# Performance work log

Hardware: AMD Instinct MI355X
Metric: run time of the kernel (lower is better)

## Reference

```python
import jax, jax.numpy as jnp
from jax import lax
import numpy as np

KSIZE = 3
STRIDE = 1
PAD = 1
SOFTMAX_SCALE = 10.0
EPS = 1e-4


def _unfold(x, k, stride, pad):
    # x: [B, C, H, W] -> ([B, L, C, k, k], Ho, Wo)  (matches torch nn.Unfold ordering)
    B, C, H, W = x.shape
    xp = jnp.pad(x, ((0, 0), (0, 0), (pad, pad), (pad, pad)))
    Ho = (H + 2 * pad - k) // stride + 1
    Wo = (W + 2 * pad - k) // stride + 1
    cols = jnp.stack(
        [xp[:, :, i:i + Ho * stride:stride, j:j + Wo * stride:stride]
         for i in range(k) for j in range(k)], axis=2)  # [B, C, k*k, Ho, Wo]
    cols = cols.reshape(B, C, k, k, Ho * Wo)
    return cols.transpose(0, 4, 1, 2, 3), Ho, Wo


def setup_inputs() -> dict:
    key = jax.random.key(0)
    kb, kf, km = jax.random.split(key, 3)
    b = jax.random.normal(kb, (4, 64, 64, 64), dtype=jnp.float32)
    f = jax.random.normal(kf, (4, 64, 64, 64), dtype=jnp.float32)
    mask = jax.random.uniform(km, (4, 1, 256, 256), dtype=jnp.float32)
    return {"b": b, "f": f, "mask": mask}


def reference(b, f, mask):
    B, C, H, W = f.shape
    k = KSIZE
    # background patches: [B, L, C, k, k]
    bp, _, _ = _unfold(b, k, STRIDE, PAD)
    # mask: avg_pool2d(kernel=4, stride=mask_scale) with mask_scale = mask.W // f.W = 4
    mp = mask.reshape(B, 1, H, 4, W, 4).mean(axis=(3, 5))  # [B, 1, H, W]
    m_unf, _, _ = _unfold(mp, k, STRIDE, PAD)  # [B, L, 1, k, k]
    m0 = m_unf[0]  # quirk of original code: first sample's mask patches used for all
    w = bp * m0[None]  # masked background patches [B, L, C, k, k]
    f_masked = f * (1.0 - mp)
    # L2 norm over (C, k, k) per patch
    norm = jnp.sqrt(jnp.sum(w * w, axis=(2, 3, 4), keepdims=True) + EPS)
    wn = w / norm
    # cosine-similarity score: conv2d(f_masked, wn) as a GEMM over unfolded f
    fp, Ho, Wo = _unfold(f_masked, k, STRIDE, PAD)  # [B, Q, C, k, k]
    score = jnp.einsum('bqcij,blcij->blq', fp, wn).reshape(B, -1, Ho, Wo)  # [B, L, Ho, Wo]
    attn = jax.nn.softmax(score * SOFTMAX_SCALE, axis=1)
    offsets = jnp.argmax(score, axis=1)[:, None]  # [B, 1, Ho, Wo]
    # conv_transpose2d(attn, w, padding=1) == conv2d with spatially flipped, channel-swapped kernel
    pad_ct = k - 1 - 1

    def _ct(a, w_i):  # a: [L, Ho, Wo], w_i: [L, C, k, k]
        kern = jnp.flip(w_i, axis=(-2, -1)).transpose(1, 0, 2, 3)  # [C, L, k, k]
        return lax.conv_general_dilated(
            a[None], kern, (1, 1), [(pad_ct, pad_ct), (pad_ct, pad_ct)],
            dimension_numbers=('NCHW', 'OIHW', 'NCHW'))[0]

    y = jax.vmap(_ct)(attn, w)  # [B, C, Ho, Wo]
    return y, offsets
```

## Files before the change

### kernel.cpp

```cpp
#include <hip/hip_runtime.h>
#include <math.h>

typedef unsigned int u32;
typedef unsigned short u16;
typedef unsigned long long u64;
typedef _Float16 h8v __attribute__((ext_vector_type(8)));
typedef float f4v __attribute__((ext_vector_type(4)));
typedef u32 u4v __attribute__((ext_vector_type(4)));

#define B_ 4
#define C_ 64
#define HW 4096
#define L_ 4096
#define D_ 576
#define MW 256
#define SCALE 10.0f
#define EPS 1e-4f
#define TAU 0.015f
#define PAIRCAP 262144

__device__ __forceinline__ u16 f16b(float x) {
  union { _Float16 h; u16 u; } c; c.h = (_Float16)x; return c.u;
}
__device__ __forceinline__ float f16f(u16 v) {
  union { u16 u; _Float16 h; } c; c.u = v; return (float)c.h;
}

__device__ __forceinline__ void gld16(const void* g, void* l) {
  __builtin_amdgcn_global_load_lds((const __attribute__((address_space(1))) void*)g,
                                   (__attribute__((address_space(3))) void*)l, 16, 0, 0);
}

__global__ __launch_bounds__(256) void k_mp(const float* __restrict__ mask, float* __restrict__ mp) {
  int idx = blockIdx.x * 256 + threadIdx.x;
  int b = idx >> 12, p = idx & 4095;
  int y = p >> 6, x = p & 63;
  const float* mb = mask + (size_t)b * MW * MW;
  float s = 0.f;
  #pragma unroll
  for (int i = 0; i < 4; ++i)
    #pragma unroll
    for (int j = 0; j < 4; ++j)
      s += mb[(y * 4 + i) * MW + x * 4 + j];
  mp[idx] = s * (1.f / 16.f);
}

__global__ __launch_bounds__(256) void k_pre2(const float* __restrict__ f, const float* __restrict__ mp,
                                              float* __restrict__ m0, float* __restrict__ fm) {
  int blk = blockIdx.x;
  if (blk < 144) {
    int idx = blk * 256 + threadIdx.x;
    int l = idx / 9, t = idx - l * 9;
    int ly = l >> 6, lx = l & 63;
    int i = t / 3, j = t - i * 3;
    int yy = ly + i - 1, xx = lx + j - 1;
    float v = 0.f;
    if ((unsigned)yy < 64u && (unsigned)xx < 64u) v = mp[(yy << 6) + xx];
    m0[idx] = v;
  } else {
    int idx = (blk - 144) * 256 + threadIdx.x;
    int p = idx & 4095;
    int b = idx >> 18;
    fm[idx] = f[idx] * (1.f - mp[(b << 12) + p]);
  }
}

__device__ __forceinline__ float patch_val(const float* __restrict__ img, const float* __restrict__ m0,
                                           int l, int d) {
  int c = d / 9, t = d - c * 9;
  int ly = l >> 6, lx = l & 63;
  int i = t / 3, j = t - i * 3;
  int yy = ly + i - 1, xx = lx + j - 1;
  float v = 0.f;
  if ((unsigned)yy < 64u && (unsigned)xx < 64u) {
    v = img[(c << 12) + (yy << 6) + xx];
    if (m0) v *= m0[l * 9 + t];
  }
  return v;
}

__global__ __launch_bounds__(256) void k_prep(const float* __restrict__ bimg, const float* __restrict__ fmb,
                                              const float* __restrict__ m0,
                                              u16* __restrict__ w_h, u16* __restrict__ fp_h,
                                              u16* __restrict__ wT_h,
                                              double* __restrict__ norme, float* __restrict__ normv,
                                              int* __restrict__ rcount, int* __restrict__ pcount,
                                              u64* __restrict__ rbest) {
  int blk = blockIdx.x;
  if (blk < 4608) {
    int gid = blk * 256 + threadIdx.x;
    int idx = gid * 2;
    int l = idx / D_, d = idx - l * D_;
    u32 h0 = f16b(patch_val(bimg, m0, l, d));
    u32 h1 = f16b(patch_val(bimg, m0, l, d + 1));
    ((u32*)w_h)[gid] = h0 | (h1 << 16);
  } else if (blk < 5632) {
    int l = (blk - 4608) * 4 + (threadIdx.x >> 6);
    int lane = threadIdx.x & 63;
    int ly = l >> 6, lx = l & 63;
    double s = 0.0;
    for (int i = lane; i < D_; i += 64) {
      int c = i / 9, t = i - c * 9;
      int ii = t / 3, jj = t - ii * 3;
      int yy = ly + ii - 1, xx = lx + jj - 1;
      if ((unsigned)yy < 64u && (unsigned)xx < 64u) {
        float wv = bimg[(c << 12) + (yy << 6) + xx] * m0[l * 9 + t];
        s += (double)wv * (double)wv;
      }
    }
    #pragma unroll
    for (int off = 32; off; off >>= 1) s += __shfl_down(s, off);
    if (lane == 0) {
      double n = sqrt(s + (double)EPS);
      norme[l] = n; normv[l] = (float)n;
    }
  } else if (blk < 10752) {
    int gid = (blk - 5632) * 256 + threadIdx.x;
    int idx = gid * 2;
    int d = idx >> 12, l = idx & 4095;
    float v0 = 0.f, v1 = 0.f;
    if (d < D_) {
      v0 = patch_val(bimg, m0, l, d);
      v1 = patch_val(bimg, m0, l + 1, d);
    }
    ((u32*)wT_h)[gid] = (u32)f16b(v0) | ((u32)f16b(v1) << 16);
  } else if (blk < 15360) {
    int gid = (blk - 10752) * 256 + threadIdx.x;
    int idx = gid * 2;
    int l = idx / D_, d = idx - l * D_;
    u32 h0 = f16b(patch_val(fmb, nullptr, l, d));
    u32 h1 = f16b(patch_val(fmb, nullptr, l, d + 1));
    ((u32*)fp_h)[gid] = h0 | (h1 << 16);
  } else {
    int e = (blk - 15360) * 256 + threadIdx.x;
    rbest[e] = 0ull;
    if (e == 0) { *rcount = 0; *pcount = 0; }
  }
}

#define STAGE1(buf, k0) do {                                                             \
    int bb = (buf) * 24576;                                                              \
    _Pragma("unroll") for (int i_ = 0; i_ < 4; ++i_) {                                   \
      int s_ = tid + i_ * 256; int r_ = s_ >> 2, ks_ = s_ & 3;                           \
      int kg_ = ks_ ^ ((r_ >> 1) & 3);                                                   \
      gld16(A + (u32)(m0 + r_) * 576u + (u32)((k0) + kg_ * 8),                           \
            (char*)lds + bb + s_ * 16); }                                                \
    _Pragma("unroll") for (int i_ = 0; i_ < 2; ++i_) {                                   \
      int s_ = tid + i_ * 256; int r_ = s_ >> 2, ks_ = s_ & 3;                           \
      int kg_ = ks_ ^ ((r_ >> 1) & 3);                                                   \
      gld16(Bm + (u32)(n0 + r_) * 576u + (u32)((k0) + kg_ * 8),                          \
            (char*)lds + bb + 16384 + s_ * 16); }                                        \
  } while (0)

__global__ __launch_bounds__(256, 2) void k_mfma1(
    const u16* __restrict__ A, const u16* __restrict__ Bm, const float* __restrict__ normv,
    u16* __restrict__ P, float* __restrict__ bm1, int* __restrict__ bi1,
    float* __restrict__ bsum, int* __restrict__ bflg)
{
  __shared__ u32 lds[18432];
  u16* ldsu = (u16*)lds;
  const int tid = threadIdx.x;
  const int lane = tid & 63, wid = tid >> 6;
  const int wrM = wid >> 1, wc = wid & 1;
  const int kq = lane >> 4, li = lane & 15;

  int nwg = gridDim.x * gridDim.y;
  int bid = blockIdx.y * gridDim.x + blockIdx.x;
  int cpx = nwg >> 3;
  int swz = (bid & 7) * cpx + (bid >> 3);
  int bx = swz % gridDim.x, by = swz / gridDim.x;
  const int m0 = by * 256, n0 = bx * 128;

  f4v acc[8][4] = {};

  STAGE1(0, 0);
  STAGE1(1, 32);

  for (int kc = 0; kc < 18; ++kc) {
    if (kc + 1 < 18) { asm volatile("s_waitcnt vmcnt(6)" ::: "memory"); }
    else             { asm volatile("s_waitcnt vmcnt(0)" ::: "memory"); }
    __builtin_amdgcn_s_barrier();
    __builtin_amdgcn_sched_barrier(0);
    if (kc + 2 < 18) STAGE1((kc + 2) % 3, (kc + 2) * 32);

    int cb = (kc % 3) * 12288;
    h8v ah[8];
    #pragma unroll
    for (int mf = 0; mf < 8; ++mf) {
      int r = wrM * 128 + mf * 16 + li;
      int off = r * 32 + (kq ^ ((r >> 1) & 3)) * 8;
      ah[mf] = *(const h8v*)&ldsu[cb + off];
    }
    #pragma unroll
    for (int nf = 0; nf < 4; ++nf) {
      int r = wc * 64 + nf * 16 + li;
      int off = r * 32 + (kq ^ ((r >> 1) & 3)) * 8;
      h8v bh = *(const h8v*)&ldsu[cb + 8192 + off];
      #pragma unroll
      for (int mf = 0; mf < 8; ++mf)
        acc[mf][nf] = __builtin_amdgcn_mfma_f32_16x16x32_f16(ah[mf], bh, acc[mf][nf], 0, 0, 0);
    }
  }
  __syncthreads();

  float* ldsf = (float*)lds;
  int*   ldsi = (int*)lds;

  float invn4[4];
  #pragma unroll
  for (int nf = 0; nf < 4; ++nf) invn4[nf] = 1.0f / normv[n0 + wc * 64 + nf * 16 + li];
  #pragma unroll
  for (int mf = 0; mf < 8; ++mf)
    #pragma unroll
    for (int nf = 0; nf < 4; ++nf)
      #pragma unroll
      for (int rr = 0; rr < 4; ++rr)
        acc[mf][nf][rr] *= invn4[nf];

  #pragma unroll
  for (int mf = 0; mf < 8; ++mf)
    #pragma unroll
    for (int rr = 0; rr < 4; ++rr) {
      int row = wrM * 128 + mf * 16 + kq * 4 + rr;
      float tv = fmaxf(fmaxf(acc[mf][0][rr], acc[mf][1][rr]), fmaxf(acc[mf][2][rr], acc[mf][3][rr]));
      ldsf[row * 33 + wc * 16 + li] = tv;
    }
  __syncthreads();
  float rV1 = -3.4e38f;
  #pragma unroll
  for (int k = 0; k < 32; ++k) rV1 = fmaxf(rV1, ldsf[tid * 33 + k]);
  ldsf[8448 + tid] = rV1;
  ldsi[8704 + tid] = 0x7fffffff;
  ldsi[8960 + tid] = 0;
  __syncthreads();

  #pragma unroll
  for (int mf = 0; mf < 8; ++mf)
    #pragma unroll
    for (int rr = 0; rr < 4; ++rr) {
      int row = wrM * 128 + mf * 16 + kq * 4 + rr;
      float v1 = ldsf[8448 + row];
      int m = m0 + row;
      float sum4 = 0.f;
      int locmin = 0x7fffffff, loccnt = 0;
      #pragma unroll
      for (int nf = 0; nf < 4; ++nf) {
        float sv = acc[mf][nf][rr];
        int n = n0 + wc * 64 + nf * 16 + li;
        float p = __expf((sv - v1) * SCALE);
        P[(u32)m * 4096u + (u32)n] = f16b(p);
        sum4 += p;
        if (sv == v1 && n < locmin) locmin = n;
        if (sv >= v1 - TAU) loccnt++;
      }
      ldsf[row * 33 + wc * 16 + li] = sum4;
      if (locmin != 0x7fffffff) atomicMin(&ldsi[8704 + row], locmin);
      if (loccnt) atomicAdd(&ldsi[8960 + row], loccnt);
    }
  __syncthreads();

  {
    float rS = 0.f;
    #pragma unroll
    for (int k = 0; k < 32; ++k) rS += ldsf[tid * 33 + k];
    int q = m0 + tid, j = n0 >> 7;
    bm1[q * 32 + j] = ldsf[8448 + tid];
    bi1[q * 32 + j] = ldsi[8704 + tid];
    bsum[q * 32 + j] = rS;
    bflg[q * 32 + j] = (ldsi[8960 + tid] >= 2) ? 1 : 0;
  }
}

__global__ __launch_bounds__(256) void k_smred(const float* __restrict__ bm1, const int* __restrict__ bi1,
                                               const float* __restrict__ bsum, const int* __restrict__ bflg,
                                               float* __restrict__ fac, float* __restrict__ gm,
                                               float* __restrict__ offs,
                                               int* __restrict__ rlist, int* __restrict__ rcount) {
  int q = blockIdx.x * 4 + (threadIdx.x >> 6);
  int lane = threadIdx.x & 63;
  if (lane >= 32) return;
  float mj = bm1[q * 32 + lane];
  int   fj = bflg[q * 32 + lane];
  float v1 = mj; int i1 = bi1[q * 32 + lane];
  #pragma unroll
  for (int d = 1; d < 32; d <<= 1) {
    float ov1 = __shfl_xor(v1, d); int oi1 = __shfl_xor(i1, d);
    if (ov1 > v1 || (ov1 == v1 && oi1 < i1)) { v1 = ov1; i1 = oi1; }
  }
  float e = __expf((mj - v1) * SCALE);
  float Z = bsum[q * 32 + lane] * e;
  #pragma unroll
  for (int d = 1; d < 32; d <<= 1) Z += __shfl_xor(Z, d);
  fac[q * 32 + lane] = e / Z;
  int jwin = i1 >> 7;
  int near = (lane != jwin) && (mj >= v1 - TAU);
  u64 bal = __ballot(near);
  int wflg = __shfl(fj, jwin);
  if (lane == 0) {
    gm[q] = v1;
    offs[q] = (float)i1;
    if (bal != 0ull || wflg) {
      int pos = atomicAdd(rcount, 1);
      if (pos < 4096) rlist[pos] = q;
    }
  }
}

__global__ __launch_bounds__(256) void k_cands(const int* __restrict__ rlist, const int* __restrict__ rcount,
                                               const u16* __restrict__ P, const float* __restrict__ bm1,
                                               const float* __restrict__ gm,
                                               u32* __restrict__ pairs, int* __restrict__ pcount) {
  __shared__ u16 pthr[32];
  int cnt = *rcount; if (cnt > 4096) cnt = 4096;
  for (int e = blockIdx.x; e < cnt; e += gridDim.x) {
    int q = rlist[e];
    float thr = gm[q] - 2.0f * TAU - 1e-3f;
    if (threadIdx.x < 32) {
      float bmj = bm1[q * 32 + threadIdx.x];
      u16 pt;
      if (bmj < thr) pt = 0x7fff;
      else {
        u16 bits = f16b(__expf((thr - bmj) * SCALE));
        pt = bits > 4 ? (u16)(bits - 4) : (u16)1;
      }
      pthr[threadIdx.x] = pt;
    }
    __syncthreads();
    int l0 = threadIdx.x * 16;
    const u4v* pr = (const u4v*)(P + (size_t)q * 4096 + l0);
    u4v a = pr[0], b2 = pr[1];
    u16 pt = pthr[threadIdx.x >> 3];
    u32 wds[8] = {a[0], a[1], a[2], a[3], b2[0], b2[1], b2[2], b2[3]};
    #pragma unroll
    for (int k = 0; k < 8; ++k) {
      u16 lo = (u16)wds[k], hi = (u16)(wds[k] >> 16);
      if (lo >= pt) {
        int pos = atomicAdd(pcount, 1);
        if (pos < PAIRCAP) pairs[pos] = ((u32)q << 12) | (u32)(l0 + 2 * k);
      }
      if (hi >= pt) {
        int pos = atomicAdd(pcount, 1);
        if (pos < PAIRCAP) pairs[pos] = ((u32)q << 12) | (u32)(l0 + 2 * k + 1);
      }
    }
    __syncthreads();
  }
}

__global__ __launch_bounds__(256) void k_attn(const u16* __restrict__ P, const float* __restrict__ fac,
                                              u16* __restrict__ attn) {
  int gid = blockIdx.x * 256 + threadIdx.x;
  u4v v = ((const u4v*)P)[gid];
  int q = gid >> 9;
  int l0 = (gid & 511) * 8;
  _Float16 fh = (_Float16)fac[q * 32 + (l0 >> 7)];
  union { u4v u; h8v h; } c; c.u = v;
  c.h *= (h8v){fh, fh, fh, fh, fh, fh, fh, fh};
  ((u4v*)attn)[gid] = c.u;
}

#define STG2(buf, k0) do {                                                               \
    int bb = (buf) * 24576;                                                              \
    _Pragma("unroll") for (int i_ = 0; i_ < 4; ++i_) {                                   \
      int s_ = tid + i_ * 256; int r_ = s_ >> 2, ks_ = s_ & 3;                           \
      int kg_ = ks_ ^ ((r_ >> 1) & 3);                                                   \
      gld16(A + (u32)(m0 + r_) * 4096u + (u32)((k0) + kg_ * 8),                          \
            (char*)lds + bb + s_ * 16); }                                                \
    _Pragma("unroll") for (int i_ = 0; i_ < 2; ++i_) {                                   \
      int s_ = tid + i_ * 256; int r_ = s_ >> 2, ks_ = s_ & 3;                           \
      int kg_ = ks_ ^ ((r_ >> 1) & 3);                                                   \
      gld16(Bm + (u32)(n0 + r_) * 4096u + (u32)((k0) + kg_ * 8),                         \
            (char*)lds + bb + 16384 + s_ * 16); }                                        \
  } while (0)

__global__ __launch_bounds__(256, 2) void k_gemm2(
    const u16* __restrict__ A, const u16* __restrict__ Bm, float* __restrict__ Gpart)
{
  __shared__ u32 lds[18432];
  u16* ldsu = (u16*)lds;
  const int tid = threadIdx.x;
  const int lane = tid & 63, wid = tid >> 6;
  const int wrM = wid >> 1, wc = wid & 1;
  const int kq = lane >> 4, li = lane & 15;

  int nwg = gridDim.x * gridDim.y;
  int bid = blockIdx.y * gridDim.x + blockIdx.x;
  int cpx = nwg >> 3;
  int swz = (bid & 7) * cpx + (bid >> 3);
  int bx = swz % gridDim.x, by = swz / gridDim.x;
  const int m0 = by * 256, n0 = bx * 128;
  const int kz = blockIdx.z * 1024;

  f4v acc[8][4] = {};

  STG2(0, kz);
  STG2(1, kz + 32);

  for (int kc = 0; kc < 32; ++kc) {
    if (kc + 1 < 32) { asm volatile("s_waitcnt vmcnt(6)" ::: "memory"); }
    else             { asm volatile("s_waitcnt vmcnt(0)" ::: "memory"); }
    __builtin_amdgcn_s_barrier();
    __builtin_amdgcn_sched_barrier(0);
    if (kc + 2 < 32) STG2((kc + 2) % 3, kz + (kc + 2) * 32);

    int cb = (kc % 3) * 12288;
    h8v ah[8];
    #pragma unroll
    for (int mf = 0; mf < 8; ++mf) {
      int r = wrM * 128 + mf * 16 + li;
      int off = r * 32 + (kq ^ ((r >> 1) & 3)) * 8;
      ah[mf] = *(const h8v*)&ldsu[cb + off];
    }
    #pragma unroll
    for (int nf = 0; nf < 4; ++nf) {
      int r = wc * 64 + nf * 16 + li;
      int off = r * 32 + (kq ^ ((r >> 1) & 3)) * 8;
      h8v bh = *(const h8v*)&ldsu[cb + 8192 + off];
      #pragma unroll
      for (int mf = 0; mf < 8; ++mf)
        acc[mf][nf] = __builtin_amdgcn_mfma_f32_16x16x32_f16(ah[mf], bh, acc[mf][nf], 0, 0, 0);
    }
  }

  float* Cf = Gpart + (size_t)blockIdx.z * 2359296;
  #pragma unroll
  for (int nf = 0; nf < 4; ++nf) {
    int n = n0 + wc * 64 + nf * 16 + li;
    if (n < D_) {
      #pragma unroll
      for (int mf = 0; mf < 8; ++mf) {
        int m = m0 + wrM * 128 + mf * 16 + kq * 4;
        *(f4v*)&Cf[(u32)n * 4096u + (u32)m] = acc[mf][nf];
      }
    }
  }
}

__global__ __launch_bounds__(256) void k_rpairs(const u32* __restrict__ pairs, const int* __restrict__ pcount,
                                                const float* __restrict__ b0, const float* __restrict__ m0,
                                                const float* __restrict__ fmb, const double* __restrict__ norme,
                                                u64* __restrict__ rbest) {
  int nw = gridDim.x * 4;
  int gw = blockIdx.x * 4 + (threadIdx.x >> 6);
  int lane = threadIdx.x & 63;
  int cnt = *pcount; if (cnt > PAIRCAP) cnt = PAIRCAP;
  for (int e = gw; e < cnt; e += nw) {
    u32 pr = pairs[e];
    int q = pr >> 12, l = pr & 4095;
    int qy = q >> 6, qx = q & 63, ly = l >> 6, lx = l & 63;
    int c = lane;
    double dot = 0.0;
    #pragma unroll
    for (int t = 0; t < 9; ++t) {
      int i = t / 3, j = t - (t / 3) * 3;
      int wy = ly + i - 1, wx = lx + j - 1;
      int fy = qy + i - 1, fx = qx + j - 1;
      float wv = 0.f, fv = 0.f;
      if ((unsigned)wy < 64u && (unsigned)wx < 64u) wv = b0[(c << 12) + (wy << 6) + wx] * m0[l * 9 + t];
      if ((unsigned)fy < 64u && (unsigned)fx < 64u) fv = fmb[(c << 12) + (fy << 6) + fx];
      dot += (double)wv * (double)fv;
    }
    #pragma unroll
    for (int off = 32; off; off >>= 1) dot += __shfl_down(dot, off);
    if (lane == 0) {
      double sc = dot / norme[l];
      u64 bbits = (u64)__double_as_longlong(sc);
      if (bbits >> 63) bbits = ~bbits; else bbits |= 0x8000000000000000ull;
      u64 key = (bbits & ~0xFFFull) | (u64)(4095 - l);
      atomicMax(rbest + q, key);
    }
  }
}

__global__ __launch_bounds__(256) void k_foldfin(const float* __restrict__ Gp, float* __restrict__ yout,
                                                 const int* __restrict__ rlist, const int* __restrict__ rcount,
                                                 const u64* __restrict__ rbest, float* __restrict__ offs) {
  if (blockIdx.x < 1024) {
    int idx = blockIdx.x * 256 + threadIdx.x;
    int c = idx >> 12, p = idx & 4095;
    int yy = p >> 6, xx = p & 63;
    float s = 0.f;
    #pragma unroll
    for (int t = 0; t < 9; ++t) {
      int i = t / 3, j = t - (t / 3) * 3;
      int qy = yy + 1 - i, qx = xx + 1 - j;
      if ((unsigned)qy < 64u && (unsigned)qx < 64u) {
        u32 base = (u32)(c * 9 + t) * 4096u + (u32)((qy << 6) + qx);
        #pragma unroll
        for (int z = 0; z < 4; ++z) s += Gp[(size_t)z * 2359296 + base];
      }
    }
    yout[idx] = s;
  } else {
    int cnt = *rcount; if (cnt > 4096) cnt = 4096;
    int e = (blockIdx.x - 1024) * 256 + threadIdx.x;
    if (e < cnt) {
      int q = rlist[e];
      offs[q] = (float)(4095 - (int)(rbest[q] & 0xFFFull));
    }
  }
}

extern "C" void kernel_launch(void* const* d_in, const int* in_sizes, int n_in,
                              void* d_out, int out_size, void* d_ws, size_t ws_size,
                              hipStream_t stream) {
  const float* b_in = (const float*)d_in[0];
  const float* f_in = (const float*)d_in[1];
  const float* mask = (const float*)d_in[2];
  float* out = (float*)d_out;

  char* ws = (char*)d_ws;
  float*  mp     = (float*)(ws + 0);
  float*  m0buf  = (float*)(ws + 65536);
  float*  fm     = (float*)(ws + 212992);
  float*  normv  = (float*)(ws + 4407296);
  double* norme  = (double*)(ws + 4423680);
  u16*    w_h    = (u16*)(ws + 4456448);
  u16*    fp_h   = (u16*)(ws + 9175040);
  u16*    wT_h   = (u16*)(ws + 13893632);
  u16*    P      = (u16*)(ws + 19136512);
  u16*    attn   = (u16*)(ws + 52690944);
  float*  bm1    = (float*)(ws + 86245376);
  int*    bi1    = (int*)(ws + 86769664);
  float*  bsum   = (float*)(ws + 87293952);
  int*    bflg   = (int*)(ws + 87818240);
  float*  fac    = (float*)(ws + 88342528);
  float*  gm     = (float*)(ws + 88866816);
  float*  Gpart  = (float*)(ws + 88883200);
  int*    rcount = (int*)(ws + 126631936);
  int*    pcount = (int*)(ws + 126631940);
  int*    rlist  = (int*)(ws + 126632192);
  u64*    rbest  = (u64*)(ws + 126648576);
  u32*    pairs  = (u32*)(ws + 126681344);

  k_mp<<<64, 256, 0, stream>>>(mask, mp);
  k_pre2<<<4240, 256, 0, stream>>>(f_in, mp, m0buf, fm);

  for (int b = 0; b < B_; ++b) {
    const float* bimg = b_in + (size_t)b * C_ * HW;
    const float* fmb  = fm + (size_t)b * C_ * HW;
    float* offs_b = out + (size_t)B_ * C_ * HW + (size_t)b * HW;

    k_prep<<<15376, 256, 0, stream>>>(bimg, fmb, m0buf, w_h, fp_h, wT_h,
                                      norme, normv, rcount, pcount, rbest);
    k_mfma1<<<dim3(32, 16), 256, 0, stream>>>(fp_h, w_h, normv, P, bm1, bi1, bsum, bflg);
    k_smred<<<1024, 256, 0, stream>>>(bm1, bi1, bsum, bflg, fac, gm, offs_b, rlist, rcount);
    k_attn<<<8192, 256, 0, stream>>>(P, fac, attn);
    k_cands<<<1024, 256, 0, stream>>>(rlist, rcount, P, bm1, gm, pairs, pcount);
    k_gemm2<<<dim3(5, 16, 4), 256, 0, stream>>>(attn, wT_h, Gpart);
    k_rpairs<<<512, 256, 0, stream>>>(pairs, pcount, bimg, m0buf, fmb, norme, rbest);
    k_foldfin<<<1040, 256, 0, stream>>>(Gpart, out + (size_t)b * C_ * HW,
                                        rlist, rcount, rbest, offs_b);
  }
}
```

Baseline: 583.6 us.

## Stage image rows in LDS for patch prep and fuse candidate scan into attn scaling

Replaces the 15k-block k_prep, which gathered every patch element from global memory, with a 64-block kernel that stages three image rows of b and f_masked in LDS and builds w, fp, wT and the norms from shared memory. Separately, the candidate-pair scan (k_cands) is folded into the attention scaling kernel, which now overwrites P in place, driven by a per-row flag written by k_smred. This removes one full pass over the large P matrix and the separate attn buffer. The cost is much lower parallelism in prep (64 blocks of 512 threads with about 98KB of LDS each), and the order in which pairs are emitted changes.

```diff
diff --git a/kernel.cpp b/kernel.cpp
--- a/kernel.cpp
+++ b/kernel.cpp
@@ -65,76 +65,98 @@
   }
 }
 
-__device__ __forceinline__ float patch_val(const float* __restrict__ img, const float* __restrict__ m0,
-                                           int l, int d) {
-  int c = d / 9, t = d - c * 9;
-  int ly = l >> 6, lx = l & 63;
-  int i = t / 3, j = t - i * 3;
-  int yy = ly + i - 1, xx = lx + j - 1;
+__device__ __forceinline__ float ldsval(const float* __restrict__ s, int lloc, int c, int t) {
+  int i2 = t / 3, j2 = t - i2 * 3;
+  int xx = lloc + j2 - 1;
   float v = 0.f;
-  if ((unsigned)yy < 64u && (unsigned)xx < 64u) {
-    v = img[(c << 12) + (yy << 6) + xx];
-    if (m0) v *= m0[l * 9 + t];
-  }
+  if ((unsigned)xx < 64u) v = s[(((i2 << 6) + c) << 6) + xx];
   return v;
 }
 
-__global__ __launch_bounds__(256) void k_prep(const float* __restrict__ bimg, const float* __restrict__ fmb,
-                                              const float* __restrict__ m0,
-                                              u16* __restrict__ w_h, u16* __restrict__ fp_h,
-                                              u16* __restrict__ wT_h,
-                                              double* __restrict__ norme, float* __restrict__ normv,
-                                              int* __restrict__ rcount, int* __restrict__ pcount,
-                                              u64* __restrict__ rbest) {
-  int blk = blockIdx.x;
-  if (blk < 4608) {
-    int gid = blk * 256 + threadIdx.x;
-    int idx = gid * 2;
-    int l = idx / D_, d = idx - l * D_;
-    u32 h0 = f16b(patch_val(bimg, m0, l, d));
-    u32 h1 = f16b(patch_val(bimg, m0, l, d + 1));
-    ((u32*)w_h)[gid] = h0 | (h1 << 16);
-  } else if (blk < 5632) {
-    int l = (blk - 4608) * 4 + (threadIdx.x >> 6);
-    int lane = threadIdx.x & 63;
-    int ly = l >> 6, lx = l & 63;
-    double s = 0.0;
-    for (int i = lane; i < D_; i += 64) {
-      int c = i / 9, t = i - c * 9;
-      int ii = t / 3, jj = t - ii * 3;
-      int yy = ly + ii - 1, xx = lx + jj - 1;
-      if ((unsigned)yy < 64u && (unsigned)xx < 64u) {
-        float wv = bimg[(c << 12) + (yy << 6) + xx] * m0[l * 9 + t];
-        s += (double)wv * (double)wv;
-      }
-    }
-    #pragma unroll
-    for (int off = 32; off; off >>= 1) s += __shfl_down(s, off);
+__global__ __launch_bounds__(512) void k_prepw(const float* __restrict__ bimg, const float* __restrict__ fmb,
+                                               const float* __restrict__ m0,
+                                               u16* __restrict__ w_h, u16* __restrict__ fp_h,
+                                               u16* __restrict__ wT_h,
+                                               double* __restrict__ norme, float* __restrict__ normv,
+                                               int* __restrict__ rcount, int* __restrict__ pcount,
+                                               u64* __restrict__ rbest) {
+  if (blockIdx.x >= 64) {
+    int e = (blockIdx.x - 64) * 512 + threadIdx.x;
+    if (e < 4096) rbest[e] = 0ull;
+    if (e == 0) { *rcount = 0; *pcount = 0; }
+    return;
+  }
+  __shared__ float s_img[12288];
+  __shared__ float s_fm[12288];
+  __shared__ float m0s[576];
+  const int ly = blockIdx.x;
+  const int tid = threadIdx.x;
+
+  #pragma unroll
+  for (int i = 0; i < 6; ++i) {
+    int slot = tid + i * 512;
+    int dy = slot >> 10, rem = slot & 1023;
+    int c = rem >> 4, xq = rem & 15;
+    int yy = ly + dy - 1;
+    f4v vi = {0.f, 0.f, 0.f, 0.f}, vf = {0.f, 0.f, 0.f, 0.f};
+    if ((unsigned)yy < 64u) {
+      vi = *(const f4v*)&bimg[(c << 12) + (yy << 6) + (xq << 2)];
+      vf = *(const f4v*)&fmb[(c << 12) + (yy << 6) + (xq << 2)];
+    }
+    *(f4v*)&s_img[slot << 2] = vi;
+    *(f4v*)&s_fm[slot << 2] = vf;
+  }
+  for (int t2 = tid; t2 < 576; t2 += 512) m0s[t2] = m0[ly * 576 + t2];
+  __syncthreads();
+
+  u32* wh32 = (u32*)w_h;
+  u32* fp32p = (u32*)fp_h;
+  #pragma unroll
+  for (int i = 0; i < 36; ++i) {
+    int g2 = tid + i * 512;
+    int idx = g2 * 2;
+    int ll = idx / 576, d0 = idx - ll * 576;
+    int c0 = d0 / 9, t0 = d0 - c0 * 9;
+    int d1 = d0 + 1;
+    int c1 = d1 / 9, t1 = d1 - c1 * 9;
+    float w0 = ldsval(s_img, ll, c0, t0) * m0s[ll * 9 + t0];
+    float w1 = ldsval(s_img, ll, c1, t1) * m0s[ll * 9 + t1];
+    wh32[ly * 18432 + g2] = (u32)f16b(w0) | ((u32)f16b(w1) << 16);
+    float p0 = ldsval(s_fm, ll, c0, t0);
+    float p1 = ldsval(s_fm, ll, c1, t1);
+    fp32p[ly * 18432 + g2] = (u32)f16b(p0) | ((u32)f16b(p1) << 16);
+  }
+
+  u32* wT32 = (u32*)wT_h;
+  #pragma unroll
+  for (int i = 0; i < 36; ++i) {
+    int g2 = tid + i * 512;
+    int d = g2 >> 5, lxp = g2 & 31;
+    int c = d / 9, t = d - c * 9;
+    float w0 = ldsval(s_img, 2 * lxp, c, t) * m0s[(2 * lxp) * 9 + t];
+    float w1 = ldsval(s_img, 2 * lxp + 1, c, t) * m0s[(2 * lxp + 1) * 9 + t];
+    wT32[d * 2048 + ly * 32 + lxp] = (u32)f16b(w0) | ((u32)f16b(w1) << 16);
+  }
+
+  int wid = tid >> 6, lane = tid & 63;
+  #pragma unroll
+  for (int it = 0; it < 8; ++it) {
+    int lloc = wid * 8 + it;
+    double ss = 0.0;
+    #pragma unroll
+    for (int k = 0; k < 9; ++k) {
+      int d = lane + k * 64;
+      int c = d / 9, t = d - c * 9;
+      float wv = ldsval(s_img, lloc, c, t) * m0s[lloc * 9 + t];
+      ss += (double)wv * (double)wv;
+    }
+    #pragma unroll
+    for (int off = 32; off; off >>= 1) ss += __shfl_down(ss, off);
     if (lane == 0) {
-      double n = sqrt(s + (double)EPS);
-      norme[l] = n; normv[l] = (float)n;
-    }
-  } else if (blk < 10752) {
-    int gid = (blk - 5632) * 256 + threadIdx.x;
-    int idx = gid * 2;
-    int d = idx >> 12, l = idx & 4095;
-    float v0 = 0.f, v1 = 0.f;
-    if (d < D_) {
-      v0 = patch_val(bimg, m0, l, d);
-      v1 = patch_val(bimg, m0, l + 1, d);
-    }
-    ((u32*)wT_h)[gid] = (u32)f16b(v0) | ((u32)f16b(v1) << 16);
-  } else if (blk < 15360) {
-    int gid = (blk - 10752) * 256 + threadIdx.x;
-    int idx = gid * 2;
-    int l = idx / D_, d = idx - l * D_;
-    u32 h0 = f16b(patch_val(fmb, nullptr, l, d));
-    u32 h1 = f16b(patch_val(fmb, nullptr, l, d + 1));
-    ((u32*)fp_h)[gid] = h0 | (h1 << 16);
-  } else {
-    int e = (blk - 15360) * 256 + threadIdx.x;
-    rbest[e] = 0ull;
-    if (e == 0) { *rcount = 0; *pcount = 0; }
+      double n = sqrt(ss + (double)EPS);
+      norme[ly * 64 + lloc] = n;
+      normv[ly * 64 + lloc] = (float)n;
+    }
   }
 }
 
@@ -274,7 +296,7 @@
 __global__ __launch_bounds__(256) void k_smred(const float* __restrict__ bm1, const int* __restrict__ bi1,
                                                const float* __restrict__ bsum, const int* __restrict__ bflg,
                                                float* __restrict__ fac, float* __restrict__ gm,
-                                               float* __restrict__ offs,
+                                               float* __restrict__ offs, int* __restrict__ rflag,
                                                int* __restrict__ rlist, int* __restrict__ rcount) {
   int q = blockIdx.x * 4 + (threadIdx.x >> 6);
   int lane = threadIdx.x & 63;
@@ -299,64 +321,50 @@
   if (lane == 0) {
     gm[q] = v1;
     offs[q] = (float)i1;
-    if (bal != 0ull || wflg) {
+    int fl = (bal != 0ull || wflg) ? 1 : 0;
+    rflag[q] = fl;
+    if (fl) {
       int pos = atomicAdd(rcount, 1);
       if (pos < 4096) rlist[pos] = q;
     }
   }
 }
 
-__global__ __launch_bounds__(256) void k_cands(const int* __restrict__ rlist, const int* __restrict__ rcount,
-                                               const u16* __restrict__ P, const float* __restrict__ bm1,
+__global__ __launch_bounds__(256) void k_attnc(u16* __restrict__ P, const float* __restrict__ fac,
+                                               const int* __restrict__ rflag, const float* __restrict__ bm1,
                                                const float* __restrict__ gm,
                                                u32* __restrict__ pairs, int* __restrict__ pcount) {
-  __shared__ u16 pthr[32];
-  int cnt = *rcount; if (cnt > 4096) cnt = 4096;
-  for (int e = blockIdx.x; e < cnt; e += gridDim.x) {
-    int q = rlist[e];
-    float thr = gm[q] - 2.0f * TAU - 1e-3f;
-    if (threadIdx.x < 32) {
-      float bmj = bm1[q * 32 + threadIdx.x];
-      u16 pt;
-      if (bmj < thr) pt = 0x7fff;
-      else {
-        u16 bits = f16b(__expf((thr - bmj) * SCALE));
-        pt = bits > 4 ? (u16)(bits - 4) : (u16)1;
-      }
-      pthr[threadIdx.x] = pt;
-    }
-    __syncthreads();
-    int l0 = threadIdx.x * 16;
-    const u4v* pr = (const u4v*)(P + (size_t)q * 4096 + l0);
-    u4v a = pr[0], b2 = pr[1];
-    u16 pt = pthr[threadIdx.x >> 3];
-    u32 wds[8] = {a[0], a[1], a[2], a[3], b2[0], b2[1], b2[2], b2[3]};
-    #pragma unroll
-    for (int k = 0; k < 8; ++k) {
-      u16 lo = (u16)wds[k], hi = (u16)(wds[k] >> 16);
-      if (lo >= pt) {
-        int pos = atomicAdd(pcount, 1);
-        if (pos < PAIRCAP) pairs[pos] = ((u32)q << 12) | (u32)(l0 + 2 * k);
-      }
-      if (hi >= pt) {
-        int pos = atomicAdd(pcount, 1);
-        if (pos < PAIRCAP) pairs[pos] = ((u32)q << 12) | (u32)(l0 + 2 * k + 1);
-      }
-    }
-    __syncthreads();
-  }
-}
-
-__global__ __launch_bounds__(256) void k_attn(const u16* __restrict__ P, const float* __restrict__ fac,
-                                              u16* __restrict__ attn) {
   int gid = blockIdx.x * 256 + threadIdx.x;
-  u4v v = ((const u4v*)P)[gid];
+  u4v v = ((u4v*)P)[gid];
   int q = gid >> 9;
   int l0 = (gid & 511) * 8;
-  _Float16 fh = (_Float16)fac[q * 32 + (l0 >> 7)];
+  int j = l0 >> 7;
+
+  if (rflag[q]) {
+    float thr = gm[q] - 2.0f * TAU - 1e-3f;
+    float bmj = bm1[q * 32 + j];
+    if (bmj >= thr) {
+      u16 bits = f16b(__expf((thr - bmj) * SCALE));
+      u16 pt = bits > 4 ? (u16)(bits - 4) : (u16)1;
+      #pragma unroll
+      for (int k = 0; k < 4; ++k) {
+        u16 lo = (u16)v[k], hi = (u16)(v[k] >> 16);
+        if (lo >= pt) {
+          int pos = atomicAdd(pcount, 1);
+          if (pos < PAIRCAP) pairs[pos] = ((u32)q << 12) | (u32)(l0 + 2 * k);
+        }
+        if (hi >= pt) {
+          int pos = atomicAdd(pcount, 1);
+          if (pos < PAIRCAP) pairs[pos] = ((u32)q << 12) | (u32)(l0 + 2 * k + 1);
+        }
+      }
+    }
+  }
+
+  _Float16 fh = (_Float16)fac[q * 32 + j];
   union { u4v u; h8v h; } c; c.u = v;
   c.h *= (h8v){fh, fh, fh, fh, fh, fh, fh, fh};
-  ((u4v*)attn)[gid] = c.u;
+  ((u4v*)P)[gid] = c.u;
 }
 
 #define STG2(buf, k0) do {                                                               \
@@ -519,7 +527,7 @@
   u16*    fp_h   = (u16*)(ws + 9175040);
   u16*    wT_h   = (u16*)(ws + 13893632);
   u16*    P      = (u16*)(ws + 19136512);
-  u16*    attn   = (u16*)(ws + 52690944);
+  int*    rflag  = (int*)(ws + 52690944);
   float*  bm1    = (float*)(ws + 86245376);
   int*    bi1    = (int*)(ws + 86769664);
   float*  bsum   = (float*)(ws + 87293952);
@@ -541,13 +549,12 @@
     const float* fmb  = fm + (size_t)b * C_ * HW;
     float* offs_b = out + (size_t)B_ * C_ * HW + (size_t)b * HW;
 
-    k_prep<<<15376, 256, 0, stream>>>(bimg, fmb, m0buf, w_h, fp_h, wT_h,
-                                      norme, normv, rcount, pcount, rbest);
+    k_prepw<<<80, 512, 0, stream>>>(bimg, fmb, m0buf, w_h, fp_h, wT_h,
+                                    norme, normv, rcount, pcount, rbest);
     k_mfma1<<<dim3(32, 16), 256, 0, stream>>>(fp_h, w_h, normv, P, bm1, bi1, bsum, bflg);
-    k_smred<<<1024, 256, 0, stream>>>(bm1, bi1, bsum, bflg, fac, gm, offs_b, rlist, rcount);
-    k_attn<<<8192, 256, 0, stream>>>(P, fac, attn);
-    k_cands<<<1024, 256, 0, stream>>>(rlist, rcount, P, bm1, gm, pairs, pcount);
-    k_gemm2<<<dim3(5, 16, 4), 256, 0, stream>>>(attn, wT_h, Gpart);
+    k_smred<<<1024, 256, 0, stream>>>(bm1, bi1, bsum, bflg, fac, gm, offs_b, rflag, rlist, rcount);
+    k_attnc<<<8192, 256, 0, stream>>>(P, fac, rflag, bm1, gm, pairs, pcount);
+    k_gemm2<<<dim3(5, 16, 4), 256, 0, stream>>>(P, wT_h, Gpart);
     k_rpairs<<<512, 256, 0, stream>>>(pairs, pcount, bimg, m0buf, fmb, norme, rbest);
     k_foldfin<<<1040, 256, 0, stream>>>(Gpart, out + (size_t)b * C_ * HW,
                                         rlist, rcount, rbest, offs_b);
```

After: 584.2 us. No clear change (+0.1%).
